# Optimization experiments

Hardware: AMD Instinct MI355X
Metric: run time of the kernel (lower is better)

The kernel has to match this reference:

```python
import jax, jax.numpy as jnp
import numpy as np

N_NODES = 100000
N_EDGES = 1600000
N_FEAT = 64
HID = 64
HL = 256
N_GRAPHS = 512


def _lin(k, i, o):
    return (jax.random.normal(k, (i, o), jnp.float32) / np.sqrt(i)).astype(jnp.float32)


def setup_inputs() -> dict:
    key = jax.random.key(0)
    ks = jax.random.split(key, 20)
    inp = {
        "x": jax.random.normal(ks[0], (N_NODES, N_FEAT), jnp.float32),
        "edge_index": jax.random.randint(ks[1], (2, N_EDGES), 0, N_NODES),
        "batch": jnp.sort(jax.random.randint(ks[2], (N_NODES,), 0, N_GRAPHS)),
        "T": jax.random.normal(ks[3], (N_GRAPHS, 1), jnp.float32),
    }
    dims = [(N_FEAT, HID), (HID, HID), (HID, HID), (HID, HID)]
    for i, (di, do) in enumerate(dims):
        inp[f"wrel{i}"] = _lin(ks[4 + 3 * i], di, do)
        inp[f"brel{i}"] = jnp.zeros((do,), jnp.float32)
        inp[f"wroot{i}"] = _lin(ks[5 + 3 * i], di, do)
    inp["w1"] = _lin(ks[16], 3 * HID + 1, HL)
    inp["b1"] = jnp.zeros((HL,), jnp.float32)
    inp["w2"] = _lin(ks[17], HL, HL)
    inp["b2"] = jnp.zeros((HL,), jnp.float32)
    inp["w3"] = _lin(ks[18], HL, 1)
    inp["b3"] = jnp.zeros((1,), jnp.float32)
    return inp


def reference(x, edge_index, batch, T,
              wrel0, brel0, wroot0,
              wrel1, brel1, wroot1,
              wrel2, brel2, wroot2,
              wrel3, brel3, wroot3,
              w1, b1, w2, b2, w3, b3):
    src, dst = edge_index[0], edge_index[1]

    def conv(h, wr, br, wq):
        # PyG GraphConv: W_root h_i + W_rel * sum_{j->i} h_j + b_rel
        agg = jax.ops.segment_sum(h[src], dst, num_segments=N_NODES)
        return agg @ wr + br + h @ wq

    h = jax.nn.relu(conv(x, wrel0, brel0, wroot0))
    h = jax.nn.relu(conv(h, wrel1, brel1, wroot1))
    h = jax.nn.relu(conv(h, wrel2, brel2, wroot2))
    h = conv(h, wrel3, brel3, wroot3)  # no relu on conv2 (matches original)

    # global add / mean / max pools over graph ids
    s = jax.ops.segment_sum(h, batch, num_segments=N_GRAPHS)
    cnt = jax.ops.segment_sum(jnp.ones((N_NODES, 1), h.dtype), batch, num_segments=N_GRAPHS)
    mean = s / jnp.maximum(cnt, 1.0)
    mx = jax.ops.segment_max(h, batch, num_segments=N_GRAPHS)
    mx = jnp.where(jnp.isfinite(mx), mx, 0.0)  # empty segments -> 0

    out = jnp.concatenate([mx, mean, s, T], axis=1)  # [G, 3*HID+1]
    o = jax.nn.relu(out @ w1 + b1)
    o = jax.nn.relu(o @ w2 + b2)  # dropout is identity in eval mode
    return o @ w3 + b3
```

## Files before the change

kernel.cpp:

```cpp
#include <hip/hip_runtime.h>
#include <hip/hip_bf16.h>
#include <math.h>

#define N_NODES 100000
#define N_EDGES 1600000
#define N_FEAT 64
#define HID 64
#define HL 256
#define N_GRAPHS 512

#define BUCKET_BITS 7
#define BUCKET_SIZE 128
#define NB ((N_NODES + BUCKET_SIZE - 1) / BUCKET_SIZE)
#define LOFS_W (NB + 1)
#define CAP 3584
#define LREC_CAP 3584
#define EDGES_PER_BLOCK 4096
#define SCAT_BLOCKS ((N_EDGES + EDGES_PER_BLOCK - 1) / EDGES_PER_BLOCK)
#define F2B_BLOCKS (N_NODES * 16 / 256)
#define WPREP_BLOCKS 128
#define ZOFF ((unsigned int)N_NODES * 128u)

typedef short vbf8 __attribute__((ext_vector_type(8)));
typedef float vf4 __attribute__((ext_vector_type(4)));
typedef float vf2 __attribute__((ext_vector_type(2)));

__device__ __forceinline__ unsigned short f2b(float f) {
    unsigned int u = __float_as_uint(f);
    return (unsigned short)((u + 0x7FFFu + ((u >> 16) & 1u)) >> 16);
}
__device__ __forceinline__ float b2f(unsigned short u) {
    return __uint_as_float(((unsigned int)u) << 16);
}
__device__ __forceinline__ unsigned pk2(float lo, float hi) {
    float2 f; f.x = lo; f.y = hi;
    __hip_bfloat162 h = __float22bfloat162_rn(f);
    unsigned r;
    __builtin_memcpy(&r, &h, 4);
    return r;
}
__device__ __forceinline__ vf2 bpair(unsigned int d) {
    vf2 r;
    r.x = __uint_as_float(d << 16);
    r.y = __uint_as_float(d & 0xFFFF0000u);
    return r;
}


__global__ __launch_bounds__(256) void k_mega(
        const int* __restrict__ src, const int* __restrict__ dst,
        int* __restrict__ lofs, unsigned int* __restrict__ ebuf,
        const float4* __restrict__ x, uint2* __restrict__ xb,
        const float* __restrict__ wroot0, const float* __restrict__ wrel0,
        const float* __restrict__ wroot1, const float* __restrict__ wrel1,
        const float* __restrict__ wroot2, const float* __restrict__ wrel2,
        const float* __restrict__ wroot3, const float* __restrict__ wrel3,
        unsigned short* __restrict__ wt) {
    __shared__ int lh[NB];
    __shared__ int lsc[256];
    __shared__ unsigned lrec[EDGES_PER_BLOCK];
    int bid = blockIdx.x;
    int t = threadIdx.x;

    if (bid < SCAT_BLOCKS) {
        for (int i = t; i < NB; i += 256) lh[i] = 0;
        __syncthreads();
        int i0 = bid * EDGES_PER_BLOCK;
        int i1 = min(N_EDGES, i0 + EDGES_PER_BLOCK);
        int cnt = i1 - i0;
        for (int i = i0 + t; i < i1; i += 256)
            atomicAdd(&lh[dst[i] >> BUCKET_BITS], 1);
        __syncthreads();
        int v[4];
        int s = 0;
        int base4 = t * 4;
#pragma unroll
        for (int j = 0; j < 4; j++) {
            v[j] = (base4 + j < NB) ? lh[base4 + j] : 0;
            s += v[j];
        }
        lsc[t] = s;
        __syncthreads();
        for (int off = 1; off < 256; off <<= 1) {
            int xx = lsc[t];
            int y = (t >= off) ? lsc[t - off] : 0;
            __syncthreads();
            lsc[t] = xx + y;
            __syncthreads();
        }
        int run = lsc[t] - s;
        int* lrow = lofs + (size_t)bid * LOFS_W;
#pragma unroll
        for (int j = 0; j < 4; j++) {
            int b = base4 + j;
            if (b < NB) {
                lrow[b] = run;
                lh[b] = run;
            }
            run += v[j];
        }
        if (t == 255) lrow[NB] = cnt;
        __syncthreads();
        for (int i = i0 + t; i < i1; i += 256) {
            int sN = src[i], d = dst[i];
            int b = d >> BUCKET_BITS;
            int p = atomicAdd(&lh[b], 1);
            lrec[p] = ((unsigned)sN << 7) | (unsigned)(d & 127);
        }
        __syncthreads();
        unsigned* eb = ebuf + (size_t)bid * EDGES_PER_BLOCK;
        for (int j = t; j < cnt; j += 256) eb[j] = lrec[j];
    } else if (bid < SCAT_BLOCKS + F2B_BLOCKS) {
        int i = (bid - SCAT_BLOCKS) * 256 + t;
        if (i < N_NODES * 16) {
            float4 v = x[i];
            uint2 o;
            o.x = pk2(v.x, v.y);
            o.y = pk2(v.z, v.w);
            xb[i] = o;
        }
    } else {
        int gi = (bid - SCAT_BLOCKS - F2B_BLOCKS) * 256 + t;
        if (gi < 4 * 64 * 128) {
            int layer = gi >> 13;
            int i = gi & 8191;
            int nn = i >> 7, k = i & 127;
            const float* wr = (layer == 0) ? wroot0 : (layer == 1) ? wroot1
                             : (layer == 2) ? wroot2 : wroot3;
            const float* wl = (layer == 0) ? wrel0 : (layer == 1) ? wrel1
                             : (layer == 2) ? wrel2 : wrel3;
            float v = (k < 64) ? wr[k * 64 + nn] : wl[(k - 64) * 64 + nn];
            wt[gi] = f2b(v);
        }
    }
}


__global__ __launch_bounds__(256) void k_fscatter2(
        const unsigned int* __restrict__ ebuf, const int* __restrict__ lofs,
        int2* __restrict__ re, unsigned int* __restrict__ soff,
        unsigned short* __restrict__ hbA, unsigned short* __restrict__ hbB, int n) {
    __shared__ int rcnt[512];
    __shared__ int rbase[512];
    __shared__ int rpre[512];
    __shared__ int tsc[256];
    __shared__ unsigned lrec[LREC_CAP];
    __shared__ int lcnt[BUCKET_SIZE];
    __shared__ int sc[BUCKET_SIZE];
    __shared__ int cur[BUCKET_SIZE];
    int b = blockIdx.x;
    int n0 = b * BUCKET_SIZE;
    int t = threadIdx.x;
    if (b == 0 && t < 16) {
        uint4 z = make_uint4(0u, 0u, 0u, 0u);
        unsigned short* hp = (t < 8) ? hbA : hbB;
        ((uint4*)(hp + (size_t)N_NODES * 64))[t & 7] = z;
    }
    for (int blk = t; blk < 512; blk += 256) {
        int c = 0, ba = 0;
        if (blk < SCAT_BLOCKS) {
            const int* lr = lofs + (size_t)blk * LOFS_W + b;
            ba = lr[0];
            c = lr[1] - ba;
        }
        rcnt[blk] = c;
        rbase[blk] = ba;
    }
    __syncthreads();
    int c0 = rcnt[2 * t], c1 = rcnt[2 * t + 1];
    tsc[t] = c0 + c1;
    __syncthreads();
    for (int off = 1; off < 256; off <<= 1) {
        int xx = tsc[t];
        int y = (t >= off) ? tsc[t - off] : 0;
        __syncthreads();
        tsc[t] = xx + y;
        __syncthreads();
    }
    int ex = tsc[t] - (c0 + c1);
    rpre[2 * t] = ex;
    rpre[2 * t + 1] = ex + c0;
    __syncthreads();
    int cb = tsc[255];
    for (int blk = t; blk < SCAT_BLOCKS; blk += 256) {
        int c = rcnt[blk];
        int dsto = rpre[blk];
        const unsigned* sp = ebuf + (size_t)blk * EDGES_PER_BLOCK + rbase[blk];
        for (int j = 0; j < c; j++) lrec[dsto + j] = sp[j];
    }
    if (t < BUCKET_SIZE) lcnt[t] = 0;
    __syncthreads();
    for (int r = t; r < cb; r += 256)
        atomicAdd(&lcnt[lrec[r] & 127u], 1);
    __syncthreads();
    int v = 0, pcnt = 0;
    if (t < BUCKET_SIZE) {
        v = lcnt[t];
        pcnt = (v + 7) & ~7;
        sc[t] = pcnt;
    }
    __syncthreads();
    for (int off = 1; off < BUCKET_SIZE; off <<= 1) {
        int xx = 0;
        if (t < BUCKET_SIZE) {
            xx = sc[t];
            if (t >= off) xx += sc[t - off];
        }
        __syncthreads();
        if (t < BUCKET_SIZE) sc[t] = xx;
        __syncthreads();
    }
    if (t < BUCKET_SIZE) {
        int start = b * CAP + sc[t] - pcnt;
        if (n0 + t < n) re[n0 + t] = make_int2(start, start + v);
        cur[t] = start;
        for (int z = start + v; z < start + pcnt; z++) soff[z] = ZOFF;
    }
    __syncthreads();
    for (int r = t; r < cb; r += 256) {
        unsigned rec = lrec[r];
        int p = atomicAdd(&cur[rec & 127u], 1);
        soff[p] = rec & ~127u;
    }
}


__global__ __launch_bounds__(256) void k_agg(
    const unsigned short* __restrict__ hb, unsigned short* __restrict__ aggb,
    const int2* __restrict__ re, const unsigned int* __restrict__ soff, int n) {
    int lane = threadIdx.x & 63;
    int wv = (blockIdx.x * 256 + threadIdx.x) >> 6;
    int m = lane >> 3;
    int sl = lane & 7;
    int i = wv * 8 + m;
    if (wv * 8 >= n) return;
    int ii = min(i, n - 1);
    int2 bd = re[ii];
    int e0 = bd.x;
    int pc = (i < n) ? ((bd.y - bd.x + 7) & ~7) : 0;

    int mx = pc;
    mx = max(mx, __shfl_xor(mx, 8));
    mx = max(mx, __shfl_xor(mx, 16));
    mx = max(mx, __shfl_xor(mx, 32));

    const char* base = (const char*)hb + sl * 16;
    vf2 A[4], B[4];
#pragma unroll
    for (int f = 0; f < 4; f++) { A[f] = (vf2){0.f, 0.f}; B[f] = (vf2){0.f, 0.f}; }

    for (int it = 0; it < mx; it += 4) {
        int t0 = it, t1 = it + 1, t2 = it + 2, t3 = it + 3;
        unsigned o0 = __builtin_nontemporal_load(soff + e0 + ((t0 < pc) ? t0 : 0));
        unsigned o1 = __builtin_nontemporal_load(soff + e0 + ((t1 < pc) ? t1 : 0));
        unsigned o2 = __builtin_nontemporal_load(soff + e0 + ((t2 < pc) ? t2 : 0));
        unsigned o3 = __builtin_nontemporal_load(soff + e0 + ((t3 < pc) ? t3 : 0));
        o0 = (t0 < pc) ? o0 : ZOFF;
        o1 = (t1 < pc) ? o1 : ZOFF;
        o2 = (t2 < pc) ? o2 : ZOFF;
        o3 = (t3 < pc) ? o3 : ZOFF;
        uint4 d0 = *(const uint4*)(base + o0);
        uint4 d1 = *(const uint4*)(base + o1);
        uint4 d2 = *(const uint4*)(base + o2);
        uint4 d3 = *(const uint4*)(base + o3);
        A[0] += bpair(d0.x); A[1] += bpair(d0.y);
        A[2] += bpair(d0.z); A[3] += bpair(d0.w);
        B[0] += bpair(d1.x); B[1] += bpair(d1.y);
        B[2] += bpair(d1.z); B[3] += bpair(d1.w);
        A[0] += bpair(d2.x); A[1] += bpair(d2.y);
        A[2] += bpair(d2.z); A[3] += bpair(d2.w);
        B[0] += bpair(d3.x); B[1] += bpair(d3.y);
        B[2] += bpair(d3.z); B[3] += bpair(d3.w);
    }

    if (i < n) {
        vf2 s0 = A[0] + B[0];
        vf2 s1 = A[1] + B[1];
        vf2 s2 = A[2] + B[2];
        vf2 s3 = A[3] + B[3];
        uint4 o;
        o.x = pk2(s0.x, s0.y);
        o.y = pk2(s1.x, s1.y);
        o.z = pk2(s2.x, s2.y);
        o.w = pk2(s3.x, s3.y);
        *(uint4*)((char*)aggb + (size_t)i * 128 + sl * 16) = o;
    }
}


template <int RELU>
__global__ __launch_bounds__(256) void k_gemm(
    const unsigned short* __restrict__ hb, const unsigned short* __restrict__ aggb,
    const unsigned short* __restrict__ wt, const float* __restrict__ brel,
    unsigned short* __restrict__ hbout, int n) {
    __shared__ float sc[4][16 * 68];

    int tid = threadIdx.x;
    int w = tid >> 6, l = tid & 63;
    int lm = l & 15, q = l >> 4;
    int r0 = blockIdx.x * 64 + w * 16;

    int arow = r0 + lm;
    if (arow >= n) arow = n - 1;
    const unsigned short* ah = hb + (size_t)arow * 64 + q * 8;
    const unsigned short* aa = aggb + (size_t)arow * 64 + q * 8;
    vbf8 afr[4];
    afr[0] = *(const vbf8*)(ah);
    afr[1] = *(const vbf8*)(ah + 32);
    afr[2] = *(const vbf8*)(aa);
    afr[3] = *(const vbf8*)(aa + 32);

    vf4 acc[4];
#pragma unroll
    for (int t = 0; t < 4; t++) acc[t] = (vf4){0.f, 0.f, 0.f, 0.f};

#pragma unroll
    for (int t = 0; t < 4; t++) {
        const unsigned short* wrow = wt + (size_t)(t * 16 + lm) * 128 + q * 8;
#pragma unroll
        for (int s = 0; s < 4; s++) {
            vbf8 bfr = *(const vbf8*)(wrow + s * 32);
            acc[t] = __builtin_amdgcn_mfma_f32_16x16x32_bf16(afr[s], bfr, acc[t], 0, 0, 0);
        }
    }

    float* sw_ = sc[w];
#pragma unroll
    for (int t = 0; t < 4; t++) {
        float b = brel[t * 16 + lm];
#pragma unroll
        for (int i = 0; i < 4; i++) {
            float v = acc[t][i] + b;
            if (RELU) v = fmaxf(v, 0.f);
            sw_[(q * 4 + i) * 68 + t * 16 + lm] = v;
        }
    }
    int rr = l >> 2, cs = l & 3;
    int node = r0 + rr;
    if (node < n) {
        const float* rp = sw_ + rr * 68 + cs * 16;
        float4 v0 = *(const float4*)(rp);
        float4 v1 = *(const float4*)(rp + 4);
        float4 v2 = *(const float4*)(rp + 8);
        float4 v3 = *(const float4*)(rp + 12);
        uint4 o0, o1;
        o0.x = pk2(v0.x, v0.y);
        o0.y = pk2(v0.z, v0.w);
        o0.z = pk2(v1.x, v1.y);
        o0.w = pk2(v1.z, v1.w);
        o1.x = pk2(v2.x, v2.y);
        o1.y = pk2(v2.z, v2.w);
        o1.z = pk2(v3.x, v3.y);
        o1.w = pk2(v3.z, v3.w);
        uint4* op = (uint4*)(hbout + (size_t)node * 64 + cs * 16);
        op[0] = o0;
        op[1] = o1;
    }
}


__global__ __launch_bounds__(256) void k_poolmlp(
    const unsigned short* __restrict__ hb, const int* __restrict__ batch,
    const float* __restrict__ T, const float* __restrict__ w1,
    const float* __restrict__ b1, const float* __restrict__ w2,
    const float* __restrict__ b2, const float* __restrict__ w3,
    const float* __restrict__ b3, float* __restrict__ out, int n) {
    __shared__ float psum[4][64];
    __shared__ float pmax[4][64];
    __shared__ float sin_[200];
    __shared__ float so1[256];
    __shared__ float red[256];
    int g = blockIdx.x, t = threadIdx.x;
    int l = t & 63, c = t >> 6;

    int lo = 0, hi = n;
    while (lo < hi) { int m = (lo + hi) >> 1; if (batch[m] < g) lo = m + 1; else hi = m; }
    int s0 = lo;
    int lo2 = s0, hi2 = n;
    while (lo2 < hi2) { int m = (lo2 + hi2) >> 1; if (batch[m] < g + 1) lo2 = m + 1; else hi2 = m; }
    int s1 = lo2;

    float sa0 = 0.f, sa1 = 0.f, sa2 = 0.f, sa3 = 0.f;
    float ma0 = -INFINITY, ma1 = -INFINITY, ma2 = -INFINITY, ma3 = -INFINITY;
    int nn = s0 + c;
    for (; nn + 12 < s1; nn += 16) {
        float v0 = b2f(hb[(size_t)nn * 64 + l]);
        float v1 = b2f(hb[(size_t)(nn + 4) * 64 + l]);
        float v2 = b2f(hb[(size_t)(nn + 8) * 64 + l]);
        float v3 = b2f(hb[(size_t)(nn + 12) * 64 + l]);
        sa0 += v0; sa1 += v1; sa2 += v2; sa3 += v3;
        ma0 = fmaxf(ma0, v0); ma1 = fmaxf(ma1, v1);
        ma2 = fmaxf(ma2, v2); ma3 = fmaxf(ma3, v3);
    }
    for (; nn < s1; nn += 4) {
        float v = b2f(hb[(size_t)nn * 64 + l]);
        sa0 += v;
        ma0 = fmaxf(ma0, v);
    }
    psum[c][l] = (sa0 + sa1) + (sa2 + sa3);
    pmax[c][l] = fmaxf(fmaxf(ma0, ma1), fmaxf(ma2, ma3));
    __syncthreads();
    if (t < 64) {
        float s = (psum[0][t] + psum[1][t]) + (psum[2][t] + psum[3][t]);
        float mx = fmaxf(fmaxf(pmax[0][t], pmax[1][t]), fmaxf(pmax[2][t], pmax[3][t]));
        int cnt = s1 - s0;
        float mean = s / fmaxf((float)cnt, 1.f);
        if (cnt == 0) mx = 0.f;
        sin_[t] = mx;
        sin_[64 + t] = mean;
        sin_[128 + t] = s;
        if (t == 0) {
            sin_[192] = T[g];
#pragma unroll
            for (int z = 193; z < 200; z++) sin_[z] = 0.f;
        }
    }
    __syncthreads();

    float a = b1[t];
    {
        float wv[8];
        for (int k = 0; k < 192; k += 8) {
#pragma unroll
            for (int u = 0; u < 8; u++) wv[u] = w1[(k + u) * 256 + t];
#pragma unroll
            for (int u = 0; u < 8; u++) a += sin_[k + u] * wv[u];
        }
        a += sin_[192] * w1[192 * 256 + t];
    }
    a = fmaxf(a, 0.f);
    so1[t] = a;
    __syncthreads();

    float a2 = b2[t];
    {
        float wv[8];
        for (int k = 0; k < 256; k += 8) {
#pragma unroll
            for (int u = 0; u < 8; u++) wv[u] = w2[(k + u) * 256 + t];
#pragma unroll
            for (int u = 0; u < 8; u++) a2 += so1[k + u] * wv[u];
        }
    }
    a2 = fmaxf(a2, 0.f);
    red[t] = a2 * w3[t];
    __syncthreads();
    for (int s = 128; s > 0; s >>= 1) {
        if (t < s) red[t] += red[t + s];
        __syncthreads();
    }
    if (t == 0) out[g] = red[0] + b3[0];
}

extern "C" void kernel_launch(void* const* d_in, const int* in_sizes, int n_in,
                              void* d_out, int out_size, void* d_ws, size_t ws_size,
                              hipStream_t stream) {
    const int N = N_NODES, E = N_EDGES, G = N_GRAPHS;

    const float* x = (const float*)d_in[0];
    const int* ei = (const int*)d_in[1];
    const int* batch = (const int*)d_in[2];
    const float* T = (const float*)d_in[3];
    const float* wrel[4] = {(const float*)d_in[4], (const float*)d_in[7],
                            (const float*)d_in[10], (const float*)d_in[13]};
    const float* brel[4] = {(const float*)d_in[5], (const float*)d_in[8],
                            (const float*)d_in[11], (const float*)d_in[14]};
    const float* wroot[4] = {(const float*)d_in[6], (const float*)d_in[9],
                             (const float*)d_in[12], (const float*)d_in[15]};
    const float* w1 = (const float*)d_in[16];
    const float* b1 = (const float*)d_in[17];
    const float* w2 = (const float*)d_in[18];
    const float* b2 = (const float*)d_in[19];
    const float* w3 = (const float*)d_in[20];
    const float* b3 = (const float*)d_in[21];
    float* out = (float*)d_out;

    const int* esrc = ei;
    const int* edst = ei + E;

    char* ws = (char*)d_ws;
    size_t off = 0;
    auto alloc = [&](size_t bytes) {
        size_t r = off;
        off = (off + bytes + 255) & ~(size_t)255;
        return r;
    };
    int* lofs = (int*)(ws + alloc((size_t)SCAT_BLOCKS * LOFS_W * 4));
    int2* re = (int2*)(ws + alloc((size_t)N * 8));
    unsigned int* soff = (unsigned int*)(ws + alloc((size_t)NB * CAP * 4));
    unsigned int* ebuf = (unsigned int*)(ws + alloc((size_t)SCAT_BLOCKS * EDGES_PER_BLOCK * 4));
    unsigned short* hbA = (unsigned short*)(ws + alloc((size_t)N * 64 * 2 + 128));
    unsigned short* hbB = (unsigned short*)(ws + alloc((size_t)N * 64 * 2 + 128));
    unsigned short* aggb = (unsigned short*)(ws + alloc((size_t)N * 64 * 2));
    unsigned short* wt = (unsigned short*)(ws + alloc((size_t)4 * 64 * 128 * 2));

    k_mega<<<SCAT_BLOCKS + F2B_BLOCKS + WPREP_BLOCKS, 256, 0, stream>>>(
        esrc, edst, lofs, ebuf, (const float4*)x, (uint2*)hbA,
        wroot[0], wrel[0], wroot[1], wrel[1],
        wroot[2], wrel[2], wroot[3], wrel[3], wt);
    k_fscatter2<<<NB, 256, 0, stream>>>(ebuf, lofs, re, soff, hbA, hbB, N);

    int agg_blocks = (N + 31) / 32;
    int gemm_blocks = (N + 63) / 64;

    k_agg<<<agg_blocks, 256, 0, stream>>>(hbA, aggb, re, soff, N);
    k_gemm<1><<<gemm_blocks, 256, 0, stream>>>(hbA, aggb, wt + 0 * 8192, brel[0], hbB, N);

    k_agg<<<agg_blocks, 256, 0, stream>>>(hbB, aggb, re, soff, N);
    k_gemm<1><<<gemm_blocks, 256, 0, stream>>>(hbB, aggb, wt + 1 * 8192, brel[1], hbA, N);

    k_agg<<<agg_blocks, 256, 0, stream>>>(hbA, aggb, re, soff, N);
    k_gemm<1><<<gemm_blocks, 256, 0, stream>>>(hbA, aggb, wt + 2 * 8192, brel[2], hbB, N);

    k_agg<<<agg_blocks, 256, 0, stream>>>(hbB, aggb, re, soff, N);
    k_gemm<0><<<gemm_blocks, 256, 0, stream>>>(hbB, aggb, wt + 3 * 8192, brel[3], hbA, N);

    k_poolmlp<<<G, 256, 0, stream>>>(hbA, batch, T, w1, b1, w2, b2, w3, b3, out, N);
}
```

Baseline: 393.2 us.

## Fuse neighbor aggregation and GEMM into one per-layer kernel via LDS

Replaces the separate k_agg and k_gemm launches with a single 512-thread k_layer kernel per GraphConv layer. The aggregated features are written to a swizzled LDS tile instead of a global aggb buffer, then read back by four waves for the MFMA GEMM. This removes the global write and re-read of the aggregate and four kernel launches. The gather loop also loads four edge offsets at once as a vector, relying on the existing ZOFF padding instead of per-element masking, and the outputs use nontemporal stores. In exchange, half the waves sit idle during the GEMM phase and the larger LDS footprint may lower occupancy.

```diff
diff --git a/kernel.cpp b/kernel.cpp
--- a/kernel.cpp
+++ b/kernel.cpp
@@ -20,10 +20,12 @@
 #define F2B_BLOCKS (N_NODES * 16 / 256)
 #define WPREP_BLOCKS 128
 #define ZOFF ((unsigned int)N_NODES * 128u)
+#define FUSE_BLOCKS ((N_NODES + 63) / 64)
 
 typedef short vbf8 __attribute__((ext_vector_type(8)));
 typedef float vf4 __attribute__((ext_vector_type(4)));
 typedef float vf2 __attribute__((ext_vector_type(2)));
+typedef unsigned int vu4 __attribute__((ext_vector_type(4)));
 
 __device__ __forceinline__ unsigned short f2b(float f) {
     unsigned int u = __float_as_uint(f);
@@ -225,55 +227,51 @@
 }
 
 
-__global__ __launch_bounds__(256) void k_agg(
-    const unsigned short* __restrict__ hb, unsigned short* __restrict__ aggb,
+template <int RELU>
+__global__ __launch_bounds__(512) void k_layer(
+    const unsigned short* __restrict__ hb,
+    const unsigned short* __restrict__ wt, const float* __restrict__ brel,
+    unsigned short* __restrict__ hbout,
     const int2* __restrict__ re, const unsigned int* __restrict__ soff, int n) {
-    int lane = threadIdx.x & 63;
-    int wv = (blockIdx.x * 256 + threadIdx.x) >> 6;
-    int m = lane >> 3;
-    int sl = lane & 7;
-    int i = wv * 8 + m;
-    if (wv * 8 >= n) return;
-    int ii = min(i, n - 1);
-    int2 bd = re[ii];
-    int e0 = bd.x;
-    int pc = (i < n) ? ((bd.y - bd.x + 7) & ~7) : 0;
-
-    int mx = pc;
-    mx = max(mx, __shfl_xor(mx, 8));
-    mx = max(mx, __shfl_xor(mx, 16));
-    mx = max(mx, __shfl_xor(mx, 32));
-
-    const char* base = (const char*)hb + sl * 16;
-    vf2 A[4], B[4];
-#pragma unroll
-    for (int f = 0; f < 4; f++) { A[f] = (vf2){0.f, 0.f}; B[f] = (vf2){0.f, 0.f}; }
-
-    for (int it = 0; it < mx; it += 4) {
-        int t0 = it, t1 = it + 1, t2 = it + 2, t3 = it + 3;
-        unsigned o0 = __builtin_nontemporal_load(soff + e0 + ((t0 < pc) ? t0 : 0));
-        unsigned o1 = __builtin_nontemporal_load(soff + e0 + ((t1 < pc) ? t1 : 0));
-        unsigned o2 = __builtin_nontemporal_load(soff + e0 + ((t2 < pc) ? t2 : 0));
-        unsigned o3 = __builtin_nontemporal_load(soff + e0 + ((t3 < pc) ? t3 : 0));
-        o0 = (t0 < pc) ? o0 : ZOFF;
-        o1 = (t1 < pc) ? o1 : ZOFF;
-        o2 = (t2 < pc) ? o2 : ZOFF;
-        o3 = (t3 < pc) ? o3 : ZOFF;
-        uint4 d0 = *(const uint4*)(base + o0);
-        uint4 d1 = *(const uint4*)(base + o1);
-        uint4 d2 = *(const uint4*)(base + o2);
-        uint4 d3 = *(const uint4*)(base + o3);
-        A[0] += bpair(d0.x); A[1] += bpair(d0.y);
-        A[2] += bpair(d0.z); A[3] += bpair(d0.w);
-        B[0] += bpair(d1.x); B[1] += bpair(d1.y);
-        B[2] += bpair(d1.z); B[3] += bpair(d1.w);
-        A[0] += bpair(d2.x); A[1] += bpair(d2.y);
-        A[2] += bpair(d2.z); A[3] += bpair(d2.w);
-        B[0] += bpair(d3.x); B[1] += bpair(d3.y);
-        B[2] += bpair(d3.z); B[3] += bpair(d3.w);
-    }
-
-    if (i < n) {
+    __shared__ float scx[4][16 * 68];
+    __shared__ unsigned int agg_lds[64][32];
+
+    int tid = threadIdx.x;
+    int w = tid >> 6, l = tid & 63;
+    int r0 = blockIdx.x * 64;
+
+    {
+        int g = l >> 3;
+        int sl = l & 7;
+        int nl = w * 8 + g;
+        int i = r0 + nl;
+        int ii = min(i, n - 1);
+        int2 bd = re[ii];
+        int e0 = bd.x;
+        int cnt = (i < n) ? (bd.y - bd.x) : 0;
+        int pc4 = (cnt + 3) & ~3;
+        const char* base = (const char*)hb + sl * 16;
+
+        vf2 A[4], B[4];
+#pragma unroll
+        for (int f = 0; f < 4; f++) { A[f] = (vf2){0.f, 0.f}; B[f] = (vf2){0.f, 0.f}; }
+
+        for (int it = 0; it < pc4; it += 4) {
+            vu4 ov = __builtin_nontemporal_load((const vu4*)(soff + e0 + it));
+            uint4 d0 = *(const uint4*)(base + ov.x);
+            uint4 d1 = *(const uint4*)(base + ov.y);
+            uint4 d2 = *(const uint4*)(base + ov.z);
+            uint4 d3 = *(const uint4*)(base + ov.w);
+            A[0] += bpair(d0.x); A[1] += bpair(d0.y);
+            A[2] += bpair(d0.z); A[3] += bpair(d0.w);
+            B[0] += bpair(d1.x); B[1] += bpair(d1.y);
+            B[2] += bpair(d1.z); B[3] += bpair(d1.w);
+            A[0] += bpair(d2.x); A[1] += bpair(d2.y);
+            A[2] += bpair(d2.z); A[3] += bpair(d2.w);
+            B[0] += bpair(d3.x); B[1] += bpair(d3.y);
+            B[2] += bpair(d3.z); B[3] += bpair(d3.w);
+        }
+
         vf2 s0 = A[0] + B[0];
         vf2 s1 = A[1] + B[1];
         vf2 s2 = A[2] + B[2];
@@ -283,78 +281,69 @@
         o.y = pk2(s1.x, s1.y);
         o.z = pk2(s2.x, s2.y);
         o.w = pk2(s3.x, s3.y);
-        *(uint4*)((char*)aggb + (size_t)i * 128 + sl * 16) = o;
-    }
-}
-
-
-template <int RELU>
-__global__ __launch_bounds__(256) void k_gemm(
-    const unsigned short* __restrict__ hb, const unsigned short* __restrict__ aggb,
-    const unsigned short* __restrict__ wt, const float* __restrict__ brel,
-    unsigned short* __restrict__ hbout, int n) {
-    __shared__ float sc[4][16 * 68];
-
-    int tid = threadIdx.x;
-    int w = tid >> 6, l = tid & 63;
-    int lm = l & 15, q = l >> 4;
-    int r0 = blockIdx.x * 64 + w * 16;
-
-    int arow = r0 + lm;
-    if (arow >= n) arow = n - 1;
-    const unsigned short* ah = hb + (size_t)arow * 64 + q * 8;
-    const unsigned short* aa = aggb + (size_t)arow * 64 + q * 8;
-    vbf8 afr[4];
-    afr[0] = *(const vbf8*)(ah);
-    afr[1] = *(const vbf8*)(ah + 32);
-    afr[2] = *(const vbf8*)(aa);
-    afr[3] = *(const vbf8*)(aa + 32);
-
-    vf4 acc[4];
-#pragma unroll
-    for (int t = 0; t < 4; t++) acc[t] = (vf4){0.f, 0.f, 0.f, 0.f};
-
-#pragma unroll
-    for (int t = 0; t < 4; t++) {
-        const unsigned short* wrow = wt + (size_t)(t * 16 + lm) * 128 + q * 8;
-#pragma unroll
-        for (int s = 0; s < 4; s++) {
-            vbf8 bfr = *(const vbf8*)(wrow + s * 32);
-            acc[t] = __builtin_amdgcn_mfma_f32_16x16x32_bf16(afr[s], bfr, acc[t], 0, 0, 0);
-        }
-    }
-
-    float* sw_ = sc[w];
-#pragma unroll
-    for (int t = 0; t < 4; t++) {
-        float b = brel[t * 16 + lm];
-#pragma unroll
-        for (int i = 0; i < 4; i++) {
-            float v = acc[t][i] + b;
-            if (RELU) v = fmaxf(v, 0.f);
-            sw_[(q * 4 + i) * 68 + t * 16 + lm] = v;
-        }
-    }
-    int rr = l >> 2, cs = l & 3;
-    int node = r0 + rr;
-    if (node < n) {
-        const float* rp = sw_ + rr * 68 + cs * 16;
-        float4 v0 = *(const float4*)(rp);
-        float4 v1 = *(const float4*)(rp + 4);
-        float4 v2 = *(const float4*)(rp + 8);
-        float4 v3 = *(const float4*)(rp + 12);
-        uint4 o0, o1;
-        o0.x = pk2(v0.x, v0.y);
-        o0.y = pk2(v0.z, v0.w);
-        o0.z = pk2(v1.x, v1.y);
-        o0.w = pk2(v1.z, v1.w);
-        o1.x = pk2(v2.x, v2.y);
-        o1.y = pk2(v2.z, v2.w);
-        o1.z = pk2(v3.x, v3.y);
-        o1.w = pk2(v3.z, v3.w);
-        uint4* op = (uint4*)(hbout + (size_t)node * 64 + cs * 16);
-        op[0] = o0;
-        op[1] = o1;
+        int c16 = sl ^ (nl & 7);
+        *(uint4*)&agg_lds[nl][c16 * 4] = o;
+    }
+    __syncthreads();
+
+    if (w < 4) {
+        int lm = l & 15, q = l >> 4;
+        int row = w * 16 + lm;
+        int arow = r0 + row;
+        if (arow >= n) arow = n - 1;
+        const unsigned short* ah = hb + (size_t)arow * 64 + q * 8;
+        vbf8 afr[4];
+        afr[0] = *(const vbf8*)(ah);
+        afr[1] = *(const vbf8*)(ah + 32);
+        afr[2] = *(const vbf8*)&agg_lds[row][((q) ^ (lm & 7)) * 4];
+        afr[3] = *(const vbf8*)&agg_lds[row][((q + 4) ^ (lm & 7)) * 4];
+
+        vf4 acc[4];
+#pragma unroll
+        for (int t = 0; t < 4; t++) acc[t] = (vf4){0.f, 0.f, 0.f, 0.f};
+
+#pragma unroll
+        for (int t = 0; t < 4; t++) {
+            const unsigned short* wrow = wt + (size_t)(t * 16 + lm) * 128 + q * 8;
+#pragma unroll
+            for (int s = 0; s < 4; s++) {
+                vbf8 bfr = *(const vbf8*)(wrow + s * 32);
+                acc[t] = __builtin_amdgcn_mfma_f32_16x16x32_bf16(afr[s], bfr, acc[t], 0, 0, 0);
+            }
+        }
+
+        float* sw_ = scx[w];
+#pragma unroll
+        for (int t = 0; t < 4; t++) {
+            float b = brel[t * 16 + lm];
+#pragma unroll
+            for (int i = 0; i < 4; i++) {
+                float v = acc[t][i] + b;
+                if (RELU) v = fmaxf(v, 0.f);
+                sw_[(q * 4 + i) * 68 + t * 16 + lm] = v;
+            }
+        }
+        int rr = l >> 2, cs = l & 3;
+        int node = r0 + w * 16 + rr;
+        if (node < n) {
+            const float* rp = sw_ + rr * 68 + cs * 16;
+            float4 v0 = *(const float4*)(rp);
+            float4 v1 = *(const float4*)(rp + 4);
+            float4 v2 = *(const float4*)(rp + 8);
+            float4 v3 = *(const float4*)(rp + 12);
+            vu4 o0, o1;
+            o0.x = pk2(v0.x, v0.y);
+            o0.y = pk2(v0.z, v0.w);
+            o0.z = pk2(v1.x, v1.y);
+            o0.w = pk2(v1.z, v1.w);
+            o1.x = pk2(v2.x, v2.y);
+            o1.y = pk2(v2.z, v2.w);
+            o1.z = pk2(v3.x, v3.y);
+            o1.w = pk2(v3.z, v3.w);
+            vu4* op = (vu4*)(hbout + (size_t)node * 64 + cs * 16);
+            __builtin_nontemporal_store(o0, op);
+            __builtin_nontemporal_store(o1, op + 1);
+        }
     }
 }
 
@@ -491,7 +480,6 @@
     unsigned int* ebuf = (unsigned int*)(ws + alloc((size_t)SCAT_BLOCKS * EDGES_PER_BLOCK * 4));
     unsigned short* hbA = (unsigned short*)(ws + alloc((size_t)N * 64 * 2 + 128));
     unsigned short* hbB = (unsigned short*)(ws + alloc((size_t)N * 64 * 2 + 128));
-    unsigned short* aggb = (unsigned short*)(ws + alloc((size_t)N * 64 * 2));
     unsigned short* wt = (unsigned short*)(ws + alloc((size_t)4 * 64 * 128 * 2));
 
     k_mega<<<SCAT_BLOCKS + F2B_BLOCKS + WPREP_BLOCKS, 256, 0, stream>>>(
@@ -500,20 +488,10 @@
         wroot[2], wrel[2], wroot[3], wrel[3], wt);
     k_fscatter2<<<NB, 256, 0, stream>>>(ebuf, lofs, re, soff, hbA, hbB, N);
 
-    int agg_blocks = (N + 31) / 32;
-    int gemm_blocks = (N + 63) / 64;
-
-    k_agg<<<agg_blocks, 256, 0, stream>>>(hbA, aggb, re, soff, N);
-    k_gemm<1><<<gemm_blocks, 256, 0, stream>>>(hbA, aggb, wt + 0 * 8192, brel[0], hbB, N);
-
-    k_agg<<<agg_blocks, 256, 0, stream>>>(hbB, aggb, re, soff, N);
-    k_gemm<1><<<gemm_blocks, 256, 0, stream>>>(hbB, aggb, wt + 1 * 8192, brel[1], hbA, N);
-
-    k_agg<<<agg_blocks, 256, 0, stream>>>(hbA, aggb, re, soff, N);
-    k_gemm<1><<<gemm_blocks, 256, 0, stream>>>(hbA, aggb, wt + 2 * 8192, brel[2], hbB, N);
-
-    k_agg<<<agg_blocks, 256, 0, stream>>>(hbB, aggb, re, soff, N);
-    k_gemm<0><<<gemm_blocks, 256, 0, stream>>>(hbB, aggb, wt + 3 * 8192, brel[3], hbA, N);
+    k_layer<1><<<FUSE_BLOCKS, 512, 0, stream>>>(hbA, wt + 0 * 8192, brel[0], hbB, re, soff, N);
+    k_layer<1><<<FUSE_BLOCKS, 512, 0, stream>>>(hbB, wt + 1 * 8192, brel[1], hbA, re, soff, N);
+    k_layer<1><<<FUSE_BLOCKS, 512, 0, stream>>>(hbA, wt + 2 * 8192, brel[2], hbB, re, soff, N);
+    k_layer<0><<<FUSE_BLOCKS, 512, 0, stream>>>(hbB, wt + 3 * 8192, brel[3], hbA, re, soff, N);
 
     k_poolmlp<<<G, 256, 0, stream>>>(hbA, batch, T, w1, b1, w2, b2, w3, b3, out, N);
 }
```

After: 344.5 us. -12.4%, faster.
